# Performance work log

Measured on AMD Instinct MI355X. Metric: run time of the kernel, lower is better.

## Reference

```python
import jax, jax.numpy as jnp
import numpy as np

NUM_CLS = 80
TOPK = 100
SCORE_THR = 0.01
DOWN_RATIO = 4.0
WH_OFFSET_BASE = 16.0
BIAS_VALUE = -4.6


def conv2d(x, w, b, pad):
    # x: [B,C,H,W], w: [O,I,kh,kw] (OIHW)
    y = jax.lax.conv_general_dilated(
        x, w, window_strides=(1, 1), padding=[(pad, pad), (pad, pad)],
        dimension_numbers=("NCHW", "OIHW", "NCHW"))
    return y + b[None, :, None, None]


def pseudo_nms(heat):
    # 3x3 maxpool, stride 1, padding 1; keep only local maxima
    hmax = jax.lax.reduce_window(
        heat, -jnp.inf, jax.lax.max,
        window_dimensions=(1, 1, 3, 3), window_strides=(1, 1, 1, 1),
        padding=((0, 0), (0, 0), (1, 1), (1, 1)))
    return heat * (hmax == heat).astype(heat.dtype)


def setup_inputs() -> dict:
    key = jax.random.key(0)
    ks = jax.random.split(key, 8)
    B, C, H, W = 16, 64, 128, 128

    def w(k, o, i, kh):
        return jax.random.normal(k, (o, i, kh, kh), jnp.float32) * 0.01

    return {
        "x": jax.random.normal(ks[0], (B, C, H, W), jnp.float32),
        "cls_w1": w(ks[1], 128, 64, 3), "cls_b1": jnp.zeros((128,), jnp.float32),
        "cls_w2": w(ks[2], 128, 128, 3), "cls_b2": jnp.zeros((128,), jnp.float32),
        "cls_w3": w(ks[3], NUM_CLS, 128, 1), "cls_b3": jnp.full((NUM_CLS,), BIAS_VALUE, jnp.float32),
        "wh_w1": w(ks[4], 64, 64, 3), "wh_b1": jnp.zeros((64,), jnp.float32),
        "wh_w2": w(ks[5], 64, 64, 3), "wh_b2": jnp.zeros((64,), jnp.float32),
        "wh_w3": w(ks[6], 4, 64, 1), "wh_b3": jnp.zeros((4,), jnp.float32),
    }


def _heads(x, cls_w1, cls_b1, cls_w2, cls_b2, cls_w3, cls_b3,
           wh_w1, wh_b1, wh_w2, wh_b2, wh_w3, wh_b3):
    h = jax.nn.relu(conv2d(x, cls_w1, cls_b1, 1))
    h = jax.nn.relu(conv2d(h, cls_w2, cls_b2, 1))
    cls = conv2d(h, cls_w3, cls_b3, 0)               # [B,num_cls,H,W]
    g = jax.nn.relu(conv2d(x, wh_w1, wh_b1, 1))
    g = jax.nn.relu(conv2d(g, wh_w2, wh_b2, 1))
    wh = jax.nn.relu(conv2d(g, wh_w3, wh_b3, 0)) * WH_OFFSET_BASE  # [B,4,H,W]
    return cls, wh


def _get_bboxes(cls, wh):
    B, cat, H, W = cls.shape
    heat = pseudo_nms(jax.nn.sigmoid(cls))
    # per-class top-k over spatial locations
    flat = heat.reshape(B, cat, H * W)
    topk_scores, topk_inds = jax.lax.top_k(flat, TOPK)        # [B,cat,K]
    topk_ys = (topk_inds // W).astype(jnp.float32)
    topk_xs = (topk_inds % W).astype(jnp.float32)
    # global top-k over (cat*K) candidates
    score, ind = jax.lax.top_k(topk_scores.reshape(B, cat * TOPK), TOPK)  # [B,K]
    clses = ind // TOPK                                       # class id
    inds = jnp.take_along_axis(topk_inds.reshape(B, -1), ind, axis=1)
    ys = jnp.take_along_axis(topk_ys.reshape(B, -1), ind, axis=1) * DOWN_RATIO
    xs = jnp.take_along_axis(topk_xs.reshape(B, -1), ind, axis=1) * DOWN_RATIO
    wh_flat = wh.transpose(0, 2, 3, 1).reshape(B, H * W, 4)
    wh_g = jnp.take_along_axis(wh_flat, inds[:, :, None], axis=1)  # [B,K,4]
    bboxes = jnp.stack([xs - wh_g[..., 0], ys - wh_g[..., 1],
                        xs + wh_g[..., 2], ys + wh_g[..., 3]], axis=-1)
    out = jnp.concatenate(
        [bboxes, score[:, :, None], clses.astype(jnp.float32)[:, :, None]], axis=-1)  # [B,K,6]
    keep = score > SCORE_THR  # padded replacement for the per-image python filter
    return out, keep


def reference(x, cls_w1, cls_b1, cls_w2, cls_b2, cls_w3, cls_b3,
              wh_w1, wh_b1, wh_w2, wh_b2, wh_w3, wh_b3):
    cls, wh = _heads(x, cls_w1, cls_b1, cls_w2, cls_b2, cls_w3, cls_b3,
                     wh_w1, wh_b1, wh_w2, wh_b2, wh_w3, wh_b3)
    return _get_bboxes(cls, wh)
```

## Files before the change

kernel.cpp:

```cpp
#include <hip/hip_runtime.h>
#include <cmath>
#include <cstdint>
#include <cfloat>


#define CN_B   16
#define CN_H   128
#define CN_W   128
#define CN_HW  16384
#define CN_CLS 80
#define CN_K   100
#define NEG_SENT (-3.402823466e+38f)

__device__ __forceinline__ unsigned ordf(float v) {
    unsigned b = __float_as_uint(v);
    return (b >> 31) ? ~b : (b | 0x80000000u);
}
__device__ __forceinline__ float unordf(unsigned o) {
    return __uint_as_float((o >> 31) ? (o & 0x7fffffffu) : ~o);
}

__device__ __forceinline__ int xcd_swz(int bid, int nwg) {
    const int q = nwg >> 3, r = nwg & 7;
    const int x = bid & 7, off = bid >> 3;
    return (x < r ? x * (q + 1) : r * (q + 1) + (x - r) * q) + off;
}

__global__ __launch_bounds__(256) void wtr_k(
    const float* __restrict__ w, float* __restrict__ wt, int CI, int CO)
{
    const int e = blockIdx.x * 256 + threadIdx.x;
    const int n = CI * 9 * CO;
    if (e < n) {
        const int co = e % CO;
        const int rest = e / CO;
        wt[e] = w[(size_t)co * CI * 9 + rest];
    }
}

__global__ __launch_bounds__(256) void wtr1x1_k(
    const float* __restrict__ w, double* __restrict__ wt)
{
    const int e = blockIdx.x * 256 + threadIdx.x;
    if (e < 128 * CN_CLS) {
        const int ci = e / CN_CLS, o = e % CN_CLS;
        wt[e] = (double)w[(size_t)o * 128 + ci];
    }
}

template<int CI>
__device__ __forceinline__ void conv3x3_body(
    const float* __restrict__ in, const float* __restrict__ wt,
    const float* __restrict__ bias, float* __restrict__ out, int CO)
{
    constexpr int CC = 4;
    const int wg  = xcd_swz(blockIdx.x, gridDim.x);
    const int cob = CO >> 4;
    const int co0 = (wg % cob) * 16;
    const int tmp = wg / cob;
    const int h0  = (tmp & 15) * 8;
    const int b   = tmp >> 4;

    __shared__ float lin[CC][10][132];

    const int t   = threadIdx.x;
    const int col = t & 127;
    const int r2  = t >> 7;
    const int g   = t >> 6;
    const int ln  = t & 63;

    float acc[4][16];
#pragma unroll
    for (int j = 0; j < 4; ++j)
#pragma unroll
        for (int o = 0; o < 16; ++o) acc[j][o] = 0.f;

    for (int ci0 = 0; ci0 < CI; ci0 += CC) {
        {
            const float* base = in + (((size_t)b * CI + ci0 + g) * CN_H) * CN_W;
#pragma unroll
            for (int rr = 0; rr < 10; ++rr) {
                const int srow = h0 - 1 + rr;
                const bool rok = (unsigned)srow < (unsigned)CN_H;
                const float* src = base + srow * CN_W;
#pragma unroll
                for (int q = 0; q < 2; ++q) {
                    const int lidx = ln + 64 * q;
                    const int scol = lidx - 1;
                    lin[g][rr][lidx] =
                        (rok && (unsigned)scol < (unsigned)CN_W) ? src[scol] : 0.f;
                }
                if (ln < 2) {
                    const int lidx = 128 + ln;
                    const int scol = lidx - 1;
                    lin[g][rr][lidx] =
                        (rok && (unsigned)scol < (unsigned)CN_W) ? src[scol] : 0.f;
                }
            }
        }
        __syncthreads();
        for (int cc = 0; cc < CC; ++cc) {
            float rb[6][3];
#pragma unroll
            for (int rr = 0; rr < 6; ++rr) {
                const int lr = r2 * 4 + rr;
                rb[rr][0] = lin[cc][lr][col + 0];
                rb[rr][1] = lin[cc][lr][col + 1];
                rb[rr][2] = lin[cc][lr][col + 2];
            }
#pragma unroll
            for (int kh = 0; kh < 3; ++kh) {
#pragma unroll
                for (int kw = 0; kw < 3; ++kw) {
                    const float* wr =
                        wt + (size_t)((ci0 + cc) * 9 + kh * 3 + kw) * CO + co0;
#pragma unroll
                    for (int o = 0; o < 16; ++o) {
                        const float w = wr[o];
                        acc[0][o] = fmaf(rb[0 + kh][kw], w, acc[0][o]);
                        acc[1][o] = fmaf(rb[1 + kh][kw], w, acc[1][o]);
                        acc[2][o] = fmaf(rb[2 + kh][kw], w, acc[2][o]);
                        acc[3][o] = fmaf(rb[3 + kh][kw], w, acc[3][o]);
                    }
                }
            }
        }
        __syncthreads();
    }

#pragma unroll
    for (int j = 0; j < 4; ++j) {
        const int h = h0 + r2 * 4 + j;
#pragma unroll
        for (int o = 0; o < 16; ++o) {
            float v = acc[j][o] + bias[co0 + o];
            v = v > 0.f ? v : 0.f;
            out[(((size_t)b * CO + co0 + o) * CN_H + h) * CN_W + col] = v;
        }
    }
}

__global__ __launch_bounds__(256) void conv_a_k(
    const float* __restrict__ in, const float* __restrict__ wt,
    const float* __restrict__ bias, float* __restrict__ out, int CO)
{ conv3x3_body<64>(in, wt, bias, out, CO); }

__global__ __launch_bounds__(256) void conv_b_k(
    const float* __restrict__ in, const float* __restrict__ wt,
    const float* __restrict__ bias, float* __restrict__ out, int CO)
{ conv3x3_body<128>(in, wt, bias, out, CO); }

__global__ __launch_bounds__(256) void conv1x1_cls_k(
    const float* __restrict__ h2, const double* __restrict__ wt,
    const float* __restrict__ bias, float* __restrict__ logits)
{
    constexpr int CI = 128;
    const int wg = xcd_swz(blockIdx.x, gridDim.x);
    const int og = wg % 5;
    const int pb = wg / 5;
    const int b  = pb / 64;
    const int p  = (pb % 64) * 256 + threadIdx.x;
    const int o0 = og * 16;

    double acc[16];
#pragma unroll
    for (int o = 0; o < 16; ++o) acc[o] = 0.0;

    for (int ci = 0; ci < CI; ++ci) {
        const double v = (double)h2[((size_t)b * CI + ci) * CN_HW + p];
        const double* wr = wt + (size_t)ci * CN_CLS + o0;
#pragma unroll
        for (int o = 0; o < 16; ++o) acc[o] = fma(v, wr[o], acc[o]);
    }
#pragma unroll
    for (int o = 0; o < 16; ++o)
        logits[((size_t)b * CN_CLS + o0 + o) * CN_HW + p] =
            (float)(acc[o] + (double)bias[o0 + o]);
}

#define NMS_CAP 2048

__global__ __launch_bounds__(256) void nms_topk_k(
    const float* __restrict__ logits,
    float* __restrict__ pc_logit, int* __restrict__ pc_ind, int b0)
{
    __shared__ unsigned long long cand[NMS_CAP];
    __shared__ int   cnt;
    __shared__ float rv[4];
    __shared__ int   ri[4];
    __shared__ int   pick;

    const int bc = blockIdx.x;
    const int bl = bc / CN_CLS;
    const int c  = bc % CN_CLS;
    const int bg = b0 + bl;
    const int t  = threadIdx.x;
    const float* L = logits + (size_t)bc * CN_HW;

    if (t == 0) cnt = 0;
    __syncthreads();

    unsigned long long flags = 0;
    for (int k = 0; k < 64; ++k) {
        const int p   = t + 256 * k;
        const int row = p >> 7, cl = p & 127;
        const float c0 = L[p];
        bool mx = true;
#pragma unroll
        for (int dr = -1; dr <= 1; ++dr)
#pragma unroll
            for (int dc = -1; dc <= 1; ++dc) {
                if (dr == 0 && dc == 0) continue;
                int rr = row + dr, cc2 = cl + dc;
                if ((unsigned)rr < (unsigned)CN_H && (unsigned)cc2 < (unsigned)CN_W)
                    if (L[(rr << 7) + cc2] > c0) mx = false;
            }
        if (mx) flags |= 1ull << k;
    }

    {
        unsigned long long f = flags;
        while (f) {
            int k = __ffsll((long long)f) - 1;
            f &= f - 1;
            const int p = t + 256 * k;
            const int slot = atomicAdd(&cnt, 1);
            if (slot < NMS_CAP)
                cand[slot] = ((unsigned long long)ordf(L[p]) << 32) | (unsigned)(~p);
        }
    }
    __syncthreads();
    const int M = cnt;

    if (M >= CN_K && M <= NMS_CAP) {
        int P = 128;
        while (P < M) P <<= 1;
        for (int i = M + t; i < P; i += 256) cand[i] = 0ull;
        __syncthreads();
        for (int k = 2; k <= P; k <<= 1) {
            for (int j = k >> 1; j > 0; j >>= 1) {
                for (int n = t; n < (P >> 1); n += 256) {
                    const int i = ((n & ~(j - 1)) << 1) | (n & (j - 1));
                    const int m = i | j;
                    const unsigned long long a = cand[i], bqq = cand[m];
                    const bool up = ((i & k) == 0);
                    if (up ? (a < bqq) : (a > bqq)) { cand[i] = bqq; cand[m] = a; }
                }
                __syncthreads();
            }
        }
        if (t < CN_K) {
            const unsigned long long key = cand[t];
            const int p = (int)(~(unsigned)key) & 0xFFFF;
            pc_logit[(size_t)bg * 8000 + c * CN_K + t] = unordf((unsigned)(key >> 32));
            pc_ind  [(size_t)bg * 8000 + c * CN_K + t] = p;
        }
    } else {
        unsigned long long removed = 0;
        for (int it = 0; it < CN_K; ++it) {
            float bv = -INFINITY;
            int   bi = 0x7fffffff;
            for (int k = 0; k < 64; ++k) {
                if ((removed >> k) & 1) continue;
                const int p = t + 256 * k;
                const float v = ((flags >> k) & 1) ? L[p] : NEG_SENT;
                if (v > bv || (v == bv && p < bi)) { bv = v; bi = p; }
            }
#pragma unroll
            for (int off = 32; off; off >>= 1) {
                float ov = __shfl_down(bv, off);
                int   oi = __shfl_down(bi, off);
                if (ov > bv || (ov == bv && oi < bi)) { bv = ov; bi = oi; }
            }
            const int wid = t >> 6;
            if ((t & 63) == 0) { rv[wid] = bv; ri[wid] = bi; }
            __syncthreads();
            if (t == 0) {
                for (int wv = 1; wv < 4; ++wv)
                    if (rv[wv] > bv || (rv[wv] == bv && ri[wv] < bi)) { bv = rv[wv]; bi = ri[wv]; }
                pc_logit[(size_t)bg * 8000 + c * CN_K + it] = bv;
                pc_ind  [(size_t)bg * 8000 + c * CN_K + it] = bi;
                pick = bi;
            }
            __syncthreads();
            const int pk = pick;
            if ((pk & 255) == t) removed |= 1ull << (pk >> 8);
            __syncthreads();
        }
    }
}

__global__ __launch_bounds__(256) void global_topk_k(
    const float* __restrict__ pc_logit, const int* __restrict__ pc_ind,
    int* __restrict__ sel)
{
    constexpr int N = CN_CLS * CN_K;
    __shared__ unsigned long long keys[N];
    __shared__ unsigned long long heads[128];
    __shared__ int rcs[CN_CLS];

    const int b = blockIdx.x;
    const int t = threadIdx.x;

    for (int n = t; n < N; n += 256) {
        const float v = pc_logit[(size_t)b * N + n];
        keys[n] = ((unsigned long long)ordf(v) << 32) | (unsigned)(~n);
    }
    if (t >= CN_CLS && t < 128) heads[t] = 0ull;
    __syncthreads();
    if (t < CN_CLS) { heads[t] = keys[t * CN_K]; rcs[t] = 1; }
    __syncthreads();

    for (int it = 0; it < CN_K; ++it) {
        if (t < 64) {
            unsigned long long k0 = heads[t];
            unsigned long long k1 = heads[t + 64];
            unsigned long long bk = (k0 >= k1) ? k0 : k1;
#pragma unroll
            for (int off = 32; off; off >>= 1) {
                unsigned long long ok = __shfl_down(bk, off);
                if (ok > bk) bk = ok;
            }
            if (t == 0) {
                const int flat = (int)(~(unsigned)bk);
                const int c    = flat / CN_K;
                sel[((size_t)b * CN_K + it) * 3 + 0] = pc_ind[(size_t)b * N + flat];
                sel[((size_t)b * CN_K + it) * 3 + 1] = c;
                sel[((size_t)b * CN_K + it) * 3 + 2] = (int)(unsigned)(bk >> 32);
                const int rc = rcs[c]++;
                heads[c] = (rc < CN_K) ? keys[c * CN_K + rc] : 0ull;
            }
        }
        __syncthreads();
    }
}

__global__ __launch_bounds__(256) void whbbox_k(
    const float* __restrict__ x,
    const float* __restrict__ w1, const float* __restrict__ b1,
    const float* __restrict__ w2, const float* __restrict__ b2,
    const float* __restrict__ w3, const float* __restrict__ b3,
    const int* __restrict__ sel, float* __restrict__ out)
{
    __shared__ float xw[64][25];
    __shared__ float g1s[9][64];
    __shared__ float g2s[64];
    __shared__ float whs[4];

    const int bk = blockIdx.x;
    const int b  = bk / CN_K;
    const int k  = bk % CN_K;
    const int t  = threadIdx.x;

    const int   ind   = sel[((size_t)b * CN_K + k) * 3 + 0];
    const int   cls   = sel[((size_t)b * CN_K + k) * 3 + 1];
    const float lg    = unordf((unsigned)sel[((size_t)b * CN_K + k) * 3 + 2]);
    const int   py = ind >> 7, px = ind & 127;

    for (int e = t; e < 64 * 25; e += 256) {
        const int c = e / 25, r = e % 25;
        const int qy = py + r / 5 - 2, qx = px + r % 5 - 2;
        float v = 0.f;
        if ((unsigned)qy < (unsigned)CN_H && (unsigned)qx < (unsigned)CN_W)
            v = x[(((size_t)b * 64 + c) * CN_H + qy) * CN_W + qx];
        xw[c][r] = v;
    }
    __syncthreads();

    for (int e = t; e < 576; e += 256) {
        const int ci = e & 63, qp = e >> 6;
        const int qdy = qp / 3 - 1, qdx = qp % 3 - 1;
        const int qy = py + qdy, qx = px + qdx;
        float s = 0.f;
        if ((unsigned)qy < (unsigned)CN_H && (unsigned)qx < (unsigned)CN_W) {
            const float* wp = w1 + (size_t)ci * 64 * 9;
            for (int cj = 0; cj < 64; ++cj) {
#pragma unroll
                for (int jh = 0; jh < 3; ++jh)
#pragma unroll
                    for (int jw = 0; jw < 3; ++jw)
                        s = fmaf(xw[cj][(qdy + jh + 1) * 5 + (qdx + jw + 1)],
                                 wp[cj * 9 + jh * 3 + jw], s);
            }
            s += b1[ci];
            s = s > 0.f ? s : 0.f;
        }
        g1s[qp][ci] = s;
    }
    __syncthreads();

    if (t < 64) {
        const int oc = t;
        const float* wp = w2 + (size_t)oc * 64 * 9;
        float s = 0.f;
        for (int ci = 0; ci < 64; ++ci) {
#pragma unroll
            for (int kh = 0; kh < 3; ++kh)
#pragma unroll
                for (int kw = 0; kw < 3; ++kw)
                    s = fmaf(g1s[kh * 3 + kw][ci], wp[ci * 9 + kh * 3 + kw], s);
        }
        s += b2[oc];
        g2s[oc] = s > 0.f ? s : 0.f;
    }
    __syncthreads();

    if (t < 4) {
        float s = 0.f;
        const float* wp = w3 + (size_t)t * 64;
        for (int oc = 0; oc < 64; ++oc) s = fmaf(g2s[oc], wp[oc], s);
        s += b3[t];
        s = s > 0.f ? s : 0.f;
        whs[t] = s * 16.0f;
    }
    __syncthreads();

    if (t == 0) {
        const float score = (float)(1.0 / (1.0 + exp(-(double)lg)));
        const float ys = (float)py * 4.0f;
        const float xs = (float)px * 4.0f;
        float* row = out + ((size_t)b * CN_K + k) * 6;
        row[0] = xs - whs[0];
        row[1] = ys - whs[1];
        row[2] = xs + whs[2];
        row[3] = ys + whs[3];
        row[4] = score;
        row[5] = (float)cls;
        out[CN_B * CN_K * 6 + b * CN_K + k] = (score > 0.01f) ? 1.0f : 0.0f;
    }
}

extern "C" void kernel_launch(void* const* d_in, const int* in_sizes, int n_in,
                              void* d_out, int out_size, void* d_ws, size_t ws_size,
                              hipStream_t stream)
{
    (void)in_sizes; (void)n_in; (void)out_size;

    const float* x      = (const float*)d_in[0];
    const float* cls_w1 = (const float*)d_in[1];
    const float* cls_b1 = (const float*)d_in[2];
    const float* cls_w2 = (const float*)d_in[3];
    const float* cls_b2 = (const float*)d_in[4];
    const float* cls_w3 = (const float*)d_in[5];
    const float* cls_b3 = (const float*)d_in[6];
    const float* wh_w1  = (const float*)d_in[7];
    const float* wh_b1  = (const float*)d_in[8];
    const float* wh_w2  = (const float*)d_in[9];
    const float* wh_b2  = (const float*)d_in[10];
    const float* wh_w3  = (const float*)d_in[11];
    const float* wh_b3  = (const float*)d_in[12];
    float* out = (float*)d_out;

    const size_t SZ_PCS = 512000u, SZ_PCI = 512000u;
    const size_t SZ_WT1 = 294912u, SZ_WT2 = 589824u;
    const size_t SZ_WTC = 81920u;
    const size_t SZ_SEL = 19200u;
    const size_t PERS = SZ_PCS + SZ_PCI + SZ_WT1 + SZ_WT2 + SZ_WTC + SZ_SEL;
    const size_t PER_IMG = 16777216u;

    int Bc = 1;
    if (ws_size > PERS) {
        size_t m = (ws_size - PERS) / PER_IMG;
        Bc = (int)(m < 1 ? 1 : (m > 16 ? 16 : m));
    }

    char* ws = (char*)d_ws;
    float*  pc_s = (float*)ws;
    int*    pc_i = (int*)(ws + SZ_PCS);
    float*  wt1  = (float*)(ws + SZ_PCS + SZ_PCI);
    float*  wt2  = (float*)(ws + SZ_PCS + SZ_PCI + SZ_WT1);
    double* wtc  = (double*)(ws + SZ_PCS + SZ_PCI + SZ_WT1 + SZ_WT2);
    int*    sel  = (int*)(ws + SZ_PCS + SZ_PCI + SZ_WT1 + SZ_WT2 + SZ_WTC);
    char*   regA = ws + PERS;
    char*   regB = regA + (size_t)Bc * 8388608u;

    dim3 blk(256);

    wtr_k<<<dim3((64 * 9 * 128 + 255) / 256), blk, 0, stream>>>(cls_w1, wt1, 64, 128);
    wtr_k<<<dim3((128 * 9 * 128 + 255) / 256), blk, 0, stream>>>(cls_w2, wt2, 128, 128);
    wtr1x1_k<<<dim3((128 * CN_CLS + 255) / 256), blk, 0, stream>>>(cls_w3, wtc);

    for (int b0 = 0; b0 < CN_B; b0 += Bc) {
        const int Bcur = (CN_B - b0 < Bc) ? (CN_B - b0) : Bc;
        const float* xc = x + (size_t)b0 * 64 * CN_HW;
        float* h1     = (float*)regA;
        float* h2     = (float*)regB;
        float* logits = (float*)regA;

        conv_a_k<<<dim3(Bcur * 16 * 8), blk, 0, stream>>>(xc, wt1, cls_b1, h1, 128);
        conv_b_k<<<dim3(Bcur * 16 * 8), blk, 0, stream>>>(h1, wt2, cls_b2, h2, 128);
        conv1x1_cls_k<<<dim3(Bcur * 64 * 5), blk, 0, stream>>>(h2, wtc, cls_b3, logits);
        nms_topk_k<<<dim3(Bcur * CN_CLS), blk, 0, stream>>>(logits, pc_s, pc_i, b0);
    }

    global_topk_k<<<dim3(CN_B), blk, 0, stream>>>(pc_s, pc_i, sel);
    whbbox_k<<<dim3(CN_B * CN_K), blk, 0, stream>>>(
        x, wh_w1, wh_b1, wh_w2, wh_b2, wh_w3, wh_b3, sel, out);
}
```

Baseline: 2.500 ms.

## Compute 3x3 local-max via register sliding window with wave shuffles

Replaces the per-pixel 9-load neighbor check in the per-class NMS/top-k kernel with a row-streaming sliding window. Each wave owns 32 rows and each lane holds two columns, and horizontal neighbors come from wave shuffles. Candidates are pushed directly to shared memory as they are found. This cuts redundant global/L1 loads from 9 per pixel to roughly one vectorized float2 per pixel. The original flag-based scan moves into the fallback branch, which recomputes flags only when that rarer path runs.

```diff
diff --git a/kernel.cpp b/kernel.cpp
--- a/kernel.cpp
+++ b/kernel.cpp
@@ -200,33 +200,49 @@
     if (t == 0) cnt = 0;
     __syncthreads();
 
-    unsigned long long flags = 0;
-    for (int k = 0; k < 64; ++k) {
-        const int p   = t + 256 * k;
-        const int row = p >> 7, cl = p & 127;
-        const float c0 = L[p];
-        bool mx = true;
-#pragma unroll
-        for (int dr = -1; dr <= 1; ++dr)
-#pragma unroll
-            for (int dc = -1; dc <= 1; ++dc) {
-                if (dr == 0 && dc == 0) continue;
-                int rr = row + dr, cc2 = cl + dc;
-                if ((unsigned)rr < (unsigned)CN_H && (unsigned)cc2 < (unsigned)CN_W)
-                    if (L[(rr << 7) + cc2] > c0) mx = false;
-            }
-        if (mx) flags |= 1ull << k;
-    }
-
     {
-        unsigned long long f = flags;
-        while (f) {
-            int k = __ffsll((long long)f) - 1;
-            f &= f - 1;
-            const int p = t + 256 * k;
-            const int slot = atomicAdd(&cnt, 1);
-            if (slot < NMS_CAP)
-                cand[slot] = ((unsigned long long)ordf(L[p]) << 32) | (unsigned)(~p);
+        const int wv = t >> 6;
+        const int ln = t & 63;
+        const int r0 = wv * 32;
+        const int c0 = ln * 2;
+
+        float m2_0 = NEG_SENT, m2_1 = NEG_SENT;
+        float m1_0 = NEG_SENT, m1_1 = NEG_SENT;
+        float pv0 = 0.f, pv1 = 0.f;
+
+        for (int rr = r0 - 1; rr <= r0 + 32; ++rr) {
+            float v0 = NEG_SENT, v1 = NEG_SENT;
+            if ((unsigned)rr < (unsigned)CN_H) {
+                const float2 vv = *reinterpret_cast<const float2*>(L + (rr << 7) + c0);
+                v0 = vv.x; v1 = vv.y;
+            }
+            float lf = __shfl_up(v1, 1);
+            if (ln == 0) lf = NEG_SENT;
+            float rt = __shfl_down(v0, 1);
+            if (ln == 63) rt = NEG_SENT;
+            const float n0 = fmaxf(fmaxf(lf, v0), v1);
+            const float n1 = fmaxf(fmaxf(v0, v1), rt);
+
+            const int e = rr - 1;
+            if (e >= r0 && e < r0 + 32) {
+                const float h0 = fmaxf(fmaxf(m2_0, m1_0), n0);
+                const float h1 = fmaxf(fmaxf(m2_1, m1_1), n1);
+                if (h0 == pv0) {
+                    const int p = (e << 7) + c0;
+                    const int slot = atomicAdd(&cnt, 1);
+                    if (slot < NMS_CAP)
+                        cand[slot] = ((unsigned long long)ordf(pv0) << 32) | (unsigned)(~p);
+                }
+                if (h1 == pv1) {
+                    const int p = (e << 7) + c0 + 1;
+                    const int slot = atomicAdd(&cnt, 1);
+                    if (slot < NMS_CAP)
+                        cand[slot] = ((unsigned long long)ordf(pv1) << 32) | (unsigned)(~p);
+                }
+            }
+            m2_0 = m1_0; m2_1 = m1_1;
+            m1_0 = n0;   m1_1 = n1;
+            pv0 = v0;    pv1 = v1;
         }
     }
     __syncthreads();
@@ -256,6 +272,23 @@
             pc_ind  [(size_t)bg * 8000 + c * CN_K + t] = p;
         }
     } else {
+        unsigned long long flags = 0;
+        for (int k = 0; k < 64; ++k) {
+            const int p   = t + 256 * k;
+            const int row = p >> 7, cl = p & 127;
+            const float c0v = L[p];
+            bool mx = true;
+#pragma unroll
+            for (int dr = -1; dr <= 1; ++dr)
+#pragma unroll
+                for (int dc = -1; dc <= 1; ++dc) {
+                    if (dr == 0 && dc == 0) continue;
+                    int rr2 = row + dr, cc2 = cl + dc;
+                    if ((unsigned)rr2 < (unsigned)CN_H && (unsigned)cc2 < (unsigned)CN_W)
+                        if (L[(rr2 << 7) + cc2] > c0v) mx = false;
+                }
+            if (mx) flags |= 1ull << k;
+        }
         unsigned long long removed = 0;
         for (int it = 0; it < CN_K; ++it) {
             float bv = -INFINITY;
@@ -276,8 +309,8 @@
             if ((t & 63) == 0) { rv[wid] = bv; ri[wid] = bi; }
             __syncthreads();
             if (t == 0) {
-                for (int wv = 1; wv < 4; ++wv)
-                    if (rv[wv] > bv || (rv[wv] == bv && ri[wv] < bi)) { bv = rv[wv]; bi = ri[wv]; }
+                for (int wv2 = 1; wv2 < 4; ++wv2)
+                    if (rv[wv2] > bv || (rv[wv2] == bv && ri[wv2] < bi)) { bv = rv[wv2]; bi = ri[wv2]; }
                 pc_logit[(size_t)bg * 8000 + c * CN_K + it] = bv;
                 pc_ind  [(size_t)bg * 8000 + c * CN_K + it] = bi;
                 pick = bi;
```

Result: faster. 2.335 ms (-6.6%).
